# Kernel tuning notes

Measured on AMD Instinct MI355X. Metric: run time of the kernel, lower is better.

The kernel has to match this reference:

```python
import jax, jax.numpy as jnp
import numpy as np

NUM_STAGES = 3
EPS = 1e-6


def _l2norm(x, axis):
    return x / (EPS + jnp.linalg.norm(x, axis=axis, keepdims=True))


def _l1norm(x, axis):
    return x / (EPS + jnp.sum(x, axis=axis, keepdims=True))


def setup_inputs() -> dict:
    key = jax.random.key(0)
    k1, k2 = jax.random.split(key)
    B, C, H, W, K = 16, 512, 64, 64, 64
    feats = jax.random.normal(k1, (B, C, H, W), dtype=jnp.float32)
    # bases buffer: N(0, sqrt(2/K)) then l2-normalized along channel dim (done in reference)
    bases = jax.random.normal(k2, (1, C, K), dtype=jnp.float32) * np.sqrt(2.0 / K)
    return {"feats": feats, "bases": bases}


def reference(feats, bases):
    B, C, H, W = feats.shape
    f = feats.reshape(B, C, H * W)              # [B, C, N]
    b = _l2norm(bases, axis=1)                  # match buffer init normalization
    b = jnp.broadcast_to(b, (B, C, b.shape[2])) # [B, C, K]
    attention = None
    for _ in range(NUM_STAGES):
        attention = jnp.einsum('bcn,bck->bnk', f, b)        # [B, N, K]
        attention = jax.nn.softmax(attention, axis=2)
        attention_normed = _l1norm(attention, axis=1)
        b = jnp.einsum('bcn,bnk->bck', f, attention_normed)  # [B, C, K]
        b = _l2norm(b, axis=1)
    # EM loop runs under torch.no_grad in the original
    b = jax.lax.stop_gradient(b)
    attention = jax.lax.stop_gradient(attention)
    feats_recon = jnp.einsum('bck,bnk->bcn', b, attention)   # [B, C, N]
    return feats_recon.reshape(B, C, H, W)
```

## Files before the change

### kernel.cpp

```cpp
#include <hip/hip_runtime.h>
#include <stdint.h>

#define B_ 16
#define C_ 512
#define N_ 4096
#define K_ 64
#define NUM_STAGES 3

typedef __bf16 bf16x8 __attribute__((ext_vector_type(8)));
typedef float f32x4 __attribute__((ext_vector_type(4)));

__device__ __forceinline__ uint16_t f2bf(float x) {
  union { float f; uint32_t u; } v; v.f = x;
  uint32_t r = (v.u + 0x7FFFu + ((v.u >> 16) & 1u)) >> 16;
  return (uint16_t)r;
}

__device__ __forceinline__ void async16(const uint16_t* g, uint16_t* l) {
  __builtin_amdgcn_global_load_lds(
      (const __attribute__((address_space(1))) unsigned int*)g,
      (__attribute__((address_space(3))) unsigned int*)l, 16, 0, 0);
}

__global__ __launch_bounds__(256) void k_prep(const float* __restrict__ feats,
                                              uint16_t* __restrict__ f16,
                                              uint16_t* __restrict__ fT16) {
  __shared__ uint32_t tile[128][64];
  int b = blockIdx.z, c0 = blockIdx.y * 128, n0 = blockIdx.x * 128;
  int t = threadIdx.x;
  int rl = t >> 4;
  int g = t & 15;
  const float* src = feats + ((size_t)b * C_ + c0) * N_ + n0;
  uint16_t* dst = f16 + ((size_t)b * C_ + c0) * N_ + n0;
#pragma unroll
  for (int i = 0; i < 8; ++i) {
    int c = rl + 16 * i;
    int n8 = g * 8;
    float4 v0 = *(const float4*)(src + (size_t)c * N_ + n8);
    float4 v1 = *(const float4*)(src + (size_t)c * N_ + n8 + 4);
    uint32_t q0 = (uint32_t)f2bf(v0.x) | ((uint32_t)f2bf(v0.y) << 16);
    uint32_t q1 = (uint32_t)f2bf(v0.z) | ((uint32_t)f2bf(v0.w) << 16);
    uint32_t q2 = (uint32_t)f2bf(v1.x) | ((uint32_t)f2bf(v1.y) << 16);
    uint32_t q3 = (uint32_t)f2bf(v1.z) | ((uint32_t)f2bf(v1.w) << 16);
    *(uint4*)(dst + (size_t)c * N_ + n8) = make_uint4(q0, q1, q2, q3);
    int h = 2 * ((c >> 3) & 15);
    int base = (4 * g) ^ (h & 28);
    int p = h & 3;
    uint32_t w[4];
    w[0 ^ p] = q0; w[1 ^ p] = q1; w[2 ^ p] = q2; w[3 ^ p] = q3;
    *(uint4*)&tile[c][base] = make_uint4(w[0], w[1], w[2], w[3]);
  }
  __syncthreads();
  uint16_t* dstT = fT16 + ((size_t)b * N_ + n0) * C_ + c0;
#pragma unroll
  for (int i = 0; i < 8; ++i) {
    int n = rl + 16 * i;
    int s = n >> 1, half = (n & 1) * 16;
    int c8 = g * 8;
    uint16_t e[8];
#pragma unroll
    for (int j = 0; j < 8; ++j) {
      int c = c8 + j;
      int h = 2 * ((c >> 3) & 15);
      uint32_t u = tile[c][s ^ h];
      e[j] = (uint16_t)(u >> half);
    }
    uint32_t q0 = (uint32_t)e[0] | ((uint32_t)e[1] << 16);
    uint32_t q1 = (uint32_t)e[2] | ((uint32_t)e[3] << 16);
    uint32_t q2 = (uint32_t)e[4] | ((uint32_t)e[5] << 16);
    uint32_t q3 = (uint32_t)e[6] | ((uint32_t)e[7] << 16);
    *(uint4*)(dstT + (size_t)n * C_ + c8) = make_uint4(q0, q1, q2, q3);
  }
}

__global__ __launch_bounds__(256) void k_init_basis(const float* __restrict__ bases,
                                                    uint16_t* __restrict__ basis,
                                                    uint16_t* __restrict__ basisT) {
  int b = blockIdx.x;
  int t = threadIdx.x;
  __shared__ float red[256];
  __shared__ float inv[64];
  int k = t & 63;
  float s = 0.f;
  for (int c = (t >> 6); c < C_; c += 4) {
    float v = bases[c * K_ + k];
    s += v * v;
  }
  red[t] = s;
  __syncthreads();
  if (t < 64) {
    float tot = red[t] + red[t + 64] + red[t + 128] + red[t + 192];
    inv[t] = 1.f / (1e-6f + sqrtf(tot));
  }
  __syncthreads();
  uint16_t* ob = basis + (size_t)b * C_ * K_;
  for (int i = 0; i < (C_ * K_) / 256; ++i) {
    int idx = t + 256 * i;
    int kk = idx & 63;
    ob[idx] = f2bf(bases[idx] * inv[kk]);
  }
  uint16_t* obT = basisT + (size_t)b * K_ * C_;
  for (int i = 0; i < (C_ * K_) / 256; ++i) {
    int idx = t + 256 * i;
    int kk = idx >> 9;
    int cc = idx & 511;
    obT[idx] = f2bf(bases[cc * K_ + kk] * inv[kk]);
  }
}

__global__ __launch_bounds__(256) void k_gemm1(const uint16_t* __restrict__ fT,
                                               const uint16_t* __restrict__ basisT,
                                               uint16_t* __restrict__ attn,
                                               uint16_t* __restrict__ attnT,
                                               int write_attn) {
  __shared__ __attribute__((aligned(16))) uint16_t ldsA[64 * 64];
  __shared__ __attribute__((aligned(16))) uint16_t ldsB[64 * 64];
  int b = blockIdx.y;
  int n0 = blockIdx.x * 64;
  int t = threadIdx.x;
  int w = t >> 6, lane = t & 63, l15 = lane & 15, quad = lane >> 4;
  const uint16_t* A = fT + ((size_t)b * N_ + n0) * C_;
  const uint16_t* Bm = basisT + (size_t)b * K_ * C_;
  f32x4 acc[4] = {};
  for (int cs = 0; cs < C_; cs += 64) {
    __syncthreads();
#pragma unroll
    for (int r = 0; r < 2; ++r) {
      int e = r * 256 + t;
      int row = e >> 3, ch = e & 7;
      int sch = (ch + row) & 7;
      async16(A + (size_t)row * C_ + cs + sch * 8, ldsA + (r * 256 + (t & 192)) * 8);
    }
#pragma unroll
    for (int r = 0; r < 2; ++r) {
      int e = r * 256 + t;
      int row = e >> 3, ch = e & 7;
      int sch = (ch + row) & 7;
      async16(Bm + (size_t)row * C_ + cs + sch * 8, ldsB + (r * 256 + (t & 192)) * 8);
    }
    __syncthreads();
#pragma unroll
    for (int s = 0; s < 2; ++s) {
      int cc = s * 4 + quad;
      int ra = 16 * w + l15;
      bf16x8 af = *(const bf16x8*)(ldsA + (ra * 8 + ((cc - ra) & 7)) * 8);
#pragma unroll
      for (int t4 = 0; t4 < 4; ++t4) {
        int rb = 16 * t4 + l15;
        bf16x8 bv = *(const bf16x8*)(ldsB + (rb * 8 + ((cc - rb) & 7)) * 8);
        acc[t4] = __builtin_amdgcn_mfma_f32_16x16x32_bf16(af, bv, acc[t4], 0, 0, 0);
      }
    }
  }
  float p[4][4];
#pragma unroll
  for (int r = 0; r < 4; ++r) {
    float m = fmaxf(fmaxf(acc[0][r], acc[1][r]), fmaxf(acc[2][r], acc[3][r]));
    m = fmaxf(m, __shfl_xor(m, 1));
    m = fmaxf(m, __shfl_xor(m, 2));
    m = fmaxf(m, __shfl_xor(m, 4));
    m = fmaxf(m, __shfl_xor(m, 8));
    float s = 0.f;
#pragma unroll
    for (int t4 = 0; t4 < 4; ++t4) { p[t4][r] = __expf(acc[t4][r] - m); s += p[t4][r]; }
    s += __shfl_xor(s, 1); s += __shfl_xor(s, 2);
    s += __shfl_xor(s, 4); s += __shfl_xor(s, 8);
    float inv = 1.f / s;
#pragma unroll
    for (int t4 = 0; t4 < 4; ++t4) p[t4][r] *= inv;
  }
  if (write_attn) {
    uint16_t* oa = attn + ((size_t)b * N_ + n0 + 16 * w + quad * 4) * K_;
#pragma unroll
    for (int r = 0; r < 4; ++r) {
#pragma unroll
      for (int t4 = 0; t4 < 4; ++t4) oa[(size_t)r * K_ + 16 * t4 + l15] = f2bf(p[t4][r]);
    }
  }
#pragma unroll
  for (int t4 = 0; t4 < 4; ++t4) {
    ushort4 y;
    y.x = f2bf(p[t4][0]); y.y = f2bf(p[t4][1]);
    y.z = f2bf(p[t4][2]); y.w = f2bf(p[t4][3]);
    *(ushort4*)(attnT + ((size_t)b * K_ + 16 * t4 + l15) * N_ + n0 + 16 * w + quad * 4) = y;
  }
}

__global__ __launch_bounds__(256) void k_gemm2(const uint16_t* __restrict__ f16,
                                               const uint16_t* __restrict__ attnT,
                                               float* __restrict__ brawT) {
  __shared__ __attribute__((aligned(16))) uint16_t ldsA[32 * 64];
  __shared__ __attribute__((aligned(16))) uint16_t ldsB[64 * 64];
  int b = blockIdx.z;
  int c0 = blockIdx.x * 32;
  int slice = blockIdx.y;
  int ns0 = slice * 1024;
  int t = threadIdx.x, w = t >> 6, lane = t & 63, l15 = lane & 15, quad = lane >> 4;
  int h = w >> 1, kh = w & 1;
  const uint16_t* A = f16 + ((size_t)b * C_ + c0) * N_;
  const uint16_t* Bm = attnT + (size_t)b * K_ * N_;
  f32x4 acc[2] = {};
  for (int ns = ns0; ns < ns0 + 1024; ns += 64) {
    __syncthreads();
    {
      int row = t >> 3, ch = t & 7;
      int sch = (ch + row) & 7;
      async16(A + (size_t)row * N_ + ns + sch * 8, ldsA + (t & 192) * 8);
    }
#pragma unroll
    for (int r = 0; r < 2; ++r) {
      int e = r * 256 + t;
      int row = e >> 3, ch = e & 7;
      int sch = (ch + row) & 7;
      async16(Bm + (size_t)row * N_ + ns + sch * 8, ldsB + (r * 256 + (t & 192)) * 8);
    }
    __syncthreads();
#pragma unroll
    for (int s = 0; s < 2; ++s) {
      int cc = s * 4 + quad;
      int ra = 16 * h + l15;
      bf16x8 af = *(const bf16x8*)(ldsA + (ra * 8 + ((cc - ra) & 7)) * 8);
#pragma unroll
      for (int t2 = 0; t2 < 2; ++t2) {
        int rb = 32 * kh + 16 * t2 + l15;
        bf16x8 bv = *(const bf16x8*)(ldsB + (rb * 8 + ((cc - rb) & 7)) * 8);
        acc[t2] = __builtin_amdgcn_mfma_f32_16x16x32_bf16(af, bv, acc[t2], 0, 0, 0);
      }
    }
  }
  float* out = brawT + ((size_t)slice * B_ + b) * K_ * C_;
#pragma unroll
  for (int t2 = 0; t2 < 2; ++t2) {
    int k = 32 * kh + 16 * t2 + l15;
    float4 v = make_float4(acc[t2][0], acc[t2][1], acc[t2][2], acc[t2][3]);
    *(float4*)(out + (size_t)k * C_ + c0 + 16 * h + quad * 4) = v;
  }
}

__global__ __launch_bounds__(256) void k_l2fused(const float* __restrict__ brawT,
                                                 uint16_t* __restrict__ basisT,
                                                 uint16_t* __restrict__ basis) {
  __shared__ float red[4][128];
  __shared__ float invs[4];
  int b = blockIdx.x, kg = blockIdx.y;
  int t = threadIdx.x, lane = t & 63;
  int c4 = (t & 127) * 4;
  int khalf = t >> 7;
  float4 bs[2];
  float pr[2];
#pragma unroll
  for (int i = 0; i < 2; ++i) {
    int k = kg * 4 + khalf * 2 + i;
    float4 a = make_float4(0.f, 0.f, 0.f, 0.f);
#pragma unroll
    for (int s = 0; s < 4; ++s) {
      const float* rp = brawT + (((size_t)s * B_ + b) * K_ + k) * C_ + c4;
      float4 v = *(const float4*)rp;
      a.x += v.x; a.y += v.y; a.z += v.z; a.w += v.w;
    }
    bs[i] = a;
    pr[i] = a.x * a.x + a.y * a.y + a.z * a.z + a.w * a.w;
  }
  red[khalf * 2 + 0][t & 127] = pr[0];
  red[khalf * 2 + 1][t & 127] = pr[1];
  __syncthreads();
  {
    int g = t >> 6;
    float s = red[g][lane] + red[g][lane + 64];
    s += __shfl_xor(s, 1); s += __shfl_xor(s, 2); s += __shfl_xor(s, 4);
    s += __shfl_xor(s, 8); s += __shfl_xor(s, 16); s += __shfl_xor(s, 32);
    if (lane == 0) invs[g] = 1.f / (1e-6f + sqrtf(s));
  }
  __syncthreads();
#pragma unroll
  for (int i = 0; i < 2; ++i) {
    int kk = khalf * 2 + i;
    int k = kg * 4 + kk;
    float inv = invs[kk];
    ushort4 y;
    y.x = f2bf(bs[i].x * inv); y.y = f2bf(bs[i].y * inv);
    y.z = f2bf(bs[i].z * inv); y.w = f2bf(bs[i].w * inv);
    *(ushort4*)(basisT + ((size_t)b * K_ + k) * C_ + c4) = y;
    uint16_t* ob = basis + (size_t)b * C_ * K_ + k;
    ob[(size_t)(c4 + 0) * K_] = y.x;
    ob[(size_t)(c4 + 1) * K_] = y.y;
    ob[(size_t)(c4 + 2) * K_] = y.z;
    ob[(size_t)(c4 + 3) * K_] = y.w;
  }
}

__global__ __launch_bounds__(256) void k_recon(const uint16_t* __restrict__ attn,
                                               const uint16_t* __restrict__ basis,
                                               float* __restrict__ out) {
  __shared__ __attribute__((aligned(16))) char smem[64 * 68 * 4];
  uint16_t* ldsA = (uint16_t*)smem;
  uint16_t* ldsB = (uint16_t*)(smem + 8192);
  float* ldsT = (float*)smem;
  int b = blockIdx.z, c0 = blockIdx.y * 64, n0 = blockIdx.x * 64;
  int t = threadIdx.x, w = t >> 6, lane = t & 63, l15 = lane & 15, quad = lane >> 4;
  const uint16_t* A = attn + ((size_t)b * N_ + n0) * K_;
  const uint16_t* Bm = basis + ((size_t)b * C_ + c0) * K_;
#pragma unroll
  for (int r = 0; r < 2; ++r) {
    int e = r * 256 + t;
    int row = e >> 3, ch = e & 7, sch = (ch + row) & 7;
    async16(A + (size_t)row * K_ + sch * 8, ldsA + (r * 256 + (t & 192)) * 8);
  }
#pragma unroll
  for (int r = 0; r < 2; ++r) {
    int e = r * 256 + t;
    int row = e >> 3, ch = e & 7, sch = (ch + row) & 7;
    async16(Bm + (size_t)row * K_ + sch * 8, ldsB + (r * 256 + (t & 192)) * 8);
  }
  f32x4 acc[4] = {};
  __syncthreads();
#pragma unroll
  for (int s = 0; s < 2; ++s) {
    int cc = s * 4 + quad;
    int ra = 16 * w + l15;
    bf16x8 af = *(const bf16x8*)(ldsA + (ra * 8 + ((cc - ra) & 7)) * 8);
#pragma unroll
    for (int t4 = 0; t4 < 4; ++t4) {
      int rb = 16 * t4 + l15;
      bf16x8 bv = *(const bf16x8*)(ldsB + (rb * 8 + ((cc - rb) & 7)) * 8);
      acc[t4] = __builtin_amdgcn_mfma_f32_16x16x32_bf16(af, bv, acc[t4], 0, 0, 0);
    }
  }
  __syncthreads();
#pragma unroll
  for (int t4 = 0; t4 < 4; ++t4) {
    float4 v = make_float4(acc[t4][0], acc[t4][1], acc[t4][2], acc[t4][3]);
    *(float4*)(ldsT + (size_t)(16 * t4 + l15) * 68 + 16 * w + quad * 4) = v;
  }
  __syncthreads();
  float* op = out + ((size_t)b * C_ + c0) * N_ + n0;
  int n4 = l15 * 4;
#pragma unroll
  for (int j = 0; j < 4; ++j) {
    int c = 16 * j + 4 * w + quad;
    *(float4*)(op + (size_t)c * N_ + n4) = *(const float4*)(ldsT + (size_t)c * 68 + n4);
  }
}

extern "C" void kernel_launch(void* const* d_in, const int* in_sizes, int n_in,
                              void* d_out, int out_size, void* d_ws, size_t ws_size,
                              hipStream_t stream) {
  const float* feats = (const float*)d_in[0];
  const float* bases = (const float*)d_in[1];
  float* out = (float*)d_out;
  char* ws = (char*)d_ws;
  uint16_t* f16 = (uint16_t*)(ws);
  uint16_t* fT16 = (uint16_t*)(ws + 67108864);
  uint16_t* attn = (uint16_t*)(ws + 134217728);
  uint16_t* attnT = (uint16_t*)(ws + 142606336);
  uint16_t* basis = (uint16_t*)(ws + 150994944);
  uint16_t* basisT = (uint16_t*)(ws + 152043520);
  float* brawT = (float*)(ws + 153092096);

  k_prep<<<dim3(32, 4, 16), 256, 0, stream>>>(feats, f16, fT16);
  k_init_basis<<<16, 256, 0, stream>>>(bases, basis, basisT);
  for (int st = 0; st < NUM_STAGES; ++st) {
    k_gemm1<<<dim3(64, 16), 256, 0, stream>>>(fT16, basisT, attn, attnT,
                                              st == NUM_STAGES - 1 ? 1 : 0);
    k_gemm2<<<dim3(16, 4, 16), 256, 0, stream>>>(f16, attnT, brawT);
    k_l2fused<<<dim3(16, 16), 256, 0, stream>>>(brawT, basisT, basis);
  }
  k_recon<<<dim3(64, 8, 16), 256, 0, stream>>>(attn, basis, out);
}
```

Measured before the change: 445.5 us.

## Drop transposed feature copy; read A operand via LDS transpose loads

The prep kernel no longer builds a transposed bf16 copy of the features. It becomes a plain grid-stride fp32-to-bf16 conversion. gemm1 now loads tiles from the channel-major bf16 array and uses ds_read_b64_tr_b16 to transpose the A operand in LDS when building MFMA fragments. This cuts 64MB of writes in prep and the workspace footprint, at the cost of strided global loads in gemm1 (16B chunks spread across channel rows) and an explicit lgkmcnt wait before the MFMAs.

```diff
diff --git a/kernel.cpp b/kernel.cpp
--- a/kernel.cpp
+++ b/kernel.cpp
@@ -9,6 +9,7 @@
 
 typedef __bf16 bf16x8 __attribute__((ext_vector_type(8)));
 typedef float f32x4 __attribute__((ext_vector_type(4)));
+typedef uint32_t u32x2 __attribute__((ext_vector_type(2)));
 
 __device__ __forceinline__ uint16_t f2bf(float x) {
   union { float f; uint32_t u; } v; v.f = x;
@@ -23,53 +24,18 @@
 }
 
 __global__ __launch_bounds__(256) void k_prep(const float* __restrict__ feats,
-                                              uint16_t* __restrict__ f16,
-                                              uint16_t* __restrict__ fT16) {
-  __shared__ uint32_t tile[128][64];
-  int b = blockIdx.z, c0 = blockIdx.y * 128, n0 = blockIdx.x * 128;
-  int t = threadIdx.x;
-  int rl = t >> 4;
-  int g = t & 15;
-  const float* src = feats + ((size_t)b * C_ + c0) * N_ + n0;
-  uint16_t* dst = f16 + ((size_t)b * C_ + c0) * N_ + n0;
-#pragma unroll
-  for (int i = 0; i < 8; ++i) {
-    int c = rl + 16 * i;
-    int n8 = g * 8;
-    float4 v0 = *(const float4*)(src + (size_t)c * N_ + n8);
-    float4 v1 = *(const float4*)(src + (size_t)c * N_ + n8 + 4);
+                                              uint16_t* __restrict__ f16) {
+  const size_t total = (size_t)B_ * C_ * N_;
+  size_t i = ((size_t)blockIdx.x * 256 + threadIdx.x) * 8;
+  const size_t stride = (size_t)gridDim.x * 256 * 8;
+  for (; i < total; i += stride) {
+    float4 v0 = *(const float4*)(feats + i);
+    float4 v1 = *(const float4*)(feats + i + 4);
     uint32_t q0 = (uint32_t)f2bf(v0.x) | ((uint32_t)f2bf(v0.y) << 16);
     uint32_t q1 = (uint32_t)f2bf(v0.z) | ((uint32_t)f2bf(v0.w) << 16);
     uint32_t q2 = (uint32_t)f2bf(v1.x) | ((uint32_t)f2bf(v1.y) << 16);
     uint32_t q3 = (uint32_t)f2bf(v1.z) | ((uint32_t)f2bf(v1.w) << 16);
-    *(uint4*)(dst + (size_t)c * N_ + n8) = make_uint4(q0, q1, q2, q3);
-    int h = 2 * ((c >> 3) & 15);
-    int base = (4 * g) ^ (h & 28);
-    int p = h & 3;
-    uint32_t w[4];
-    w[0 ^ p] = q0; w[1 ^ p] = q1; w[2 ^ p] = q2; w[3 ^ p] = q3;
-    *(uint4*)&tile[c][base] = make_uint4(w[0], w[1], w[2], w[3]);
-  }
-  __syncthreads();
-  uint16_t* dstT = fT16 + ((size_t)b * N_ + n0) * C_ + c0;
-#pragma unroll
-  for (int i = 0; i < 8; ++i) {
-    int n = rl + 16 * i;
-    int s = n >> 1, half = (n & 1) * 16;
-    int c8 = g * 8;
-    uint16_t e[8];
-#pragma unroll
-    for (int j = 0; j < 8; ++j) {
-      int c = c8 + j;
-      int h = 2 * ((c >> 3) & 15);
-      uint32_t u = tile[c][s ^ h];
-      e[j] = (uint16_t)(u >> half);
-    }
-    uint32_t q0 = (uint32_t)e[0] | ((uint32_t)e[1] << 16);
-    uint32_t q1 = (uint32_t)e[2] | ((uint32_t)e[3] << 16);
-    uint32_t q2 = (uint32_t)e[4] | ((uint32_t)e[5] << 16);
-    uint32_t q3 = (uint32_t)e[6] | ((uint32_t)e[7] << 16);
-    *(uint4*)(dstT + (size_t)n * C_ + c8) = make_uint4(q0, q1, q2, q3);
+    *(uint4*)(f16 + i) = make_uint4(q0, q1, q2, q3);
   }
 }
 
@@ -108,7 +74,7 @@
   }
 }
 
-__global__ __launch_bounds__(256) void k_gemm1(const uint16_t* __restrict__ fT,
+__global__ __launch_bounds__(256) void k_gemm1(const uint16_t* __restrict__ f16,
                                                const uint16_t* __restrict__ basisT,
                                                uint16_t* __restrict__ attn,
                                                uint16_t* __restrict__ attnT,
@@ -119,17 +85,27 @@
   int n0 = blockIdx.x * 64;
   int t = threadIdx.x;
   int w = t >> 6, lane = t & 63, l15 = lane & 15, quad = lane >> 4;
-  const uint16_t* A = fT + ((size_t)b * N_ + n0) * C_;
+  const uint16_t* A = f16 + (size_t)b * C_ * N_;
   const uint16_t* Bm = basisT + (size_t)b * K_ * C_;
+  int cA[2], nA[2];
+#pragma unroll
+  for (int r = 0; r < 2; ++r) {
+    int o = r * 256 + t;
+    int ng = o >> 7, p = (o >> 3) & 15, e = o & 7;
+    int sc = (p & 8) + ((p & 3) << 1) + ((p >> 2) & 1);
+    cA[r] = 4 * sc + (e >> 1);
+    nA[r] = n0 + 16 * ng + 8 * (e & 1);
+  }
+  uint32_t aBase =
+      (uint32_t)(uintptr_t)(const __attribute__((address_space(3))) uint16_t*)ldsA;
+  uint32_t trAddr = aBase + (uint32_t)w * 2048u + (uint32_t)lane * 8u;
   f32x4 acc[4] = {};
   for (int cs = 0; cs < C_; cs += 64) {
     __syncthreads();
 #pragma unroll
     for (int r = 0; r < 2; ++r) {
-      int e = r * 256 + t;
-      int row = e >> 3, ch = e & 7;
-      int sch = (ch + row) & 7;
-      async16(A + (size_t)row * C_ + cs + sch * 8, ldsA + (r * 256 + (t & 192)) * 8);
+      async16(A + (size_t)(cs + cA[r]) * N_ + nA[r],
+              ldsA + (r * 256 + (t & 192)) * 8);
     }
 #pragma unroll
     for (int r = 0; r < 2; ++r) {
@@ -139,11 +115,20 @@
       async16(Bm + (size_t)row * C_ + cs + sch * 8, ldsB + (r * 256 + (t & 192)) * 8);
     }
     __syncthreads();
+    u32x2 q0, q1, q2, q3;
+    asm volatile("ds_read_b64_tr_b16 %0, %1" : "=v"(q0) : "v"(trAddr));
+    asm volatile("ds_read_b64_tr_b16 %0, %1 offset:512" : "=v"(q1) : "v"(trAddr));
+    asm volatile("ds_read_b64_tr_b16 %0, %1 offset:1024" : "=v"(q2) : "v"(trAddr));
+    asm volatile("ds_read_b64_tr_b16 %0, %1 offset:1536" : "=v"(q3) : "v"(trAddr));
+    asm volatile("s_waitcnt lgkmcnt(0)" ::: "memory");
+    __builtin_amdgcn_sched_barrier(0);
+    bf16x8 af0, af1;
+    ((u32x2*)&af0)[0] = q0; ((u32x2*)&af0)[1] = q1;
+    ((u32x2*)&af1)[0] = q2; ((u32x2*)&af1)[1] = q3;
 #pragma unroll
     for (int s = 0; s < 2; ++s) {
       int cc = s * 4 + quad;
-      int ra = 16 * w + l15;
-      bf16x8 af = *(const bf16x8*)(ldsA + (ra * 8 + ((cc - ra) & 7)) * 8);
+      bf16x8 af = s ? af1 : af0;
 #pragma unroll
       for (int t4 = 0; t4 < 4; ++t4) {
         int rb = 16 * t4 + l15;
@@ -350,17 +335,16 @@
   float* out = (float*)d_out;
   char* ws = (char*)d_ws;
   uint16_t* f16 = (uint16_t*)(ws);
-  uint16_t* fT16 = (uint16_t*)(ws + 67108864);
-  uint16_t* attn = (uint16_t*)(ws + 134217728);
-  uint16_t* attnT = (uint16_t*)(ws + 142606336);
-  uint16_t* basis = (uint16_t*)(ws + 150994944);
-  uint16_t* basisT = (uint16_t*)(ws + 152043520);
-  float* brawT = (float*)(ws + 153092096);
-
-  k_prep<<<dim3(32, 4, 16), 256, 0, stream>>>(feats, f16, fT16);
+  uint16_t* attn = (uint16_t*)(ws + 67108864);
+  uint16_t* attnT = (uint16_t*)(ws + 75497472);
+  uint16_t* basis = (uint16_t*)(ws + 83886080);
+  uint16_t* basisT = (uint16_t*)(ws + 84934656);
+  float* brawT = (float*)(ws + 85983232);
+
+  k_prep<<<2048, 256, 0, stream>>>(feats, f16);
   k_init_basis<<<16, 256, 0, stream>>>(bases, basis, basisT);
   for (int st = 0; st < NUM_STAGES; ++st) {
-    k_gemm1<<<dim3(64, 16), 256, 0, stream>>>(fT16, basisT, attn, attnT,
+    k_gemm1<<<dim3(64, 16), 256, 0, stream>>>(f16, basisT, attn, attnT,
                                               st == NUM_STAGES - 1 ? 1 : 0);
     k_gemm2<<<dim3(16, 4, 16), 256, 0, stream>>>(f16, attnT, brawT);
     k_l2fused<<<dim3(16, 16), 256, 0, stream>>>(brawT, basisT, basis);
```

Result: no change. 443.5 us (-0.4%).
